# Kernel tuning notes

Measured on AMD Instinct MI355X. Metric: run time of the kernel, lower is better.

The kernel has to match this reference:

```python
import jax, jax.numpy as jnp
import numpy as np

NUM_HEADS = 16
HEAD_SIZE = 64
MAX_POS = 2048  # config.max_position_embeddings


def setup_inputs() -> dict:
    key = jax.random.key(0)
    ks = jax.random.split(key, 8)
    B, Lq, Lk, D = 4, 1024, 2048, 1024
    s = 1.0 / np.sqrt(D)
    return {
        "hidden_states": jax.random.normal(ks[0], (B, Lk, D), jnp.float32),
        "query_hidden_states": jax.random.normal(ks[1], (B, Lq, D), jnp.float32),
        "attention_mask": jnp.zeros((B, 1, 1, Lk), jnp.float32),
        "Wq": jax.random.normal(ks[2], (D, D), jnp.float32) * s,
        "bq": jnp.zeros((D,), jnp.float32),
        "Wk": jax.random.normal(ks[3], (D, D), jnp.float32) * s,
        "bk": jnp.zeros((D,), jnp.float32),
        "Wv": jax.random.normal(ks[4], (D, D), jnp.float32) * s,
        "bv": jnp.zeros((D,), jnp.float32),
        "dist_emb": jax.random.normal(ks[5], (2 * MAX_POS - 1, HEAD_SIZE), jnp.float32) * 0.02,
    }


def _split_heads(x):
    # [B, L, H*Dh] -> [B, H, L, Dh]
    B, L, _ = x.shape
    return x.reshape(B, L, NUM_HEADS, HEAD_SIZE).transpose(0, 2, 1, 3)


def reference(hidden_states, query_hidden_states, attention_mask, Wq, bq, Wk, bk, Wv, bv, dist_emb):
    # Linear projections (torch Linear: x @ W.T + b)
    q = _split_heads(query_hidden_states @ Wq.T + bq)   # [B,H,Lq,Dh]
    k = _split_heads(hidden_states @ Wk.T + bk)          # [B,H,Lk,Dh]
    v = _split_heads(hidden_states @ Wv.T + bv)          # [B,H,Lk,Dh]

    scores = jnp.einsum('bhld,bhrd->bhlr', q, k)         # [B,H,Lq,Lk]

    # relative_key_query positional scores
    Lq, Lk = q.shape[2], k.shape[2]
    distance = jnp.arange(Lq)[:, None] - jnp.arange(Lk)[None, :]
    pe = dist_emb[distance + MAX_POS - 1]                # [Lq,Lk,Dh]
    scores = scores + jnp.einsum('bhld,lrd->bhlr', q, pe) + jnp.einsum('bhrd,lrd->bhlr', k, pe)

    scores = scores / np.sqrt(HEAD_SIZE) + attention_mask
    probs = jax.nn.softmax(scores, axis=-1)              # dropout p=0 (eval)
    ctx = jnp.einsum('bhlr,bhrd->bhld', probs, v)        # [B,H,Lq,Dh]
    B = ctx.shape[0]
    return ctx.transpose(0, 2, 1, 3).reshape(B, Lq, NUM_HEADS * HEAD_SIZE)
```

## Files before the change

### kernel.cpp

```cpp
#include <hip/hip_runtime.h>
#include <hip/hip_bf16.h>

#define B_   4
#define H_   16
#define LQ   1024
#define LK   2048
#define D_   1024
#define DH   64

typedef __attribute__((ext_vector_type(8))) short  short8;
typedef __attribute__((ext_vector_type(4))) float  float4_;
typedef __attribute__((ext_vector_type(4))) unsigned int uint4_;

static __device__ __forceinline__ float bf2f(unsigned short u) {
    unsigned int x = ((unsigned int)u) << 16;
    return __builtin_bit_cast(float, x);
}
static __device__ __forceinline__ unsigned short f2bf(float f) {
    unsigned int x = __builtin_bit_cast(unsigned int, f);
    unsigned int lsb = (x >> 16) & 1u;
    x += 0x7fffu + lsb;
    return (unsigned short)(x >> 16);
}
static __device__ __forceinline__ uint4_ pack8(float4_ a, float4_ b) {
    uint4_ o;
    o[0] = (unsigned int)f2bf(a[0]) | ((unsigned int)f2bf(a[1]) << 16);
    o[1] = (unsigned int)f2bf(a[2]) | ((unsigned int)f2bf(a[3]) << 16);
    o[2] = (unsigned int)f2bf(b[0]) | ((unsigned int)f2bf(b[1]) << 16);
    o[3] = (unsigned int)f2bf(b[2]) | ((unsigned int)f2bf(b[3]) << 16);
    return o;
}

#define MFMA(a, b, c) __builtin_amdgcn_mfma_f32_16x16x32_bf16((a), (b), (c), 0, 0, 0)

__global__ __launch_bounds__(256) void proj_kernel(
    const float* __restrict__ Xq, const float* __restrict__ Xk,
    const float* __restrict__ Wq, const float* __restrict__ bq,
    const float* __restrict__ Wk, const float* __restrict__ bk,
    const float* __restrict__ Wv, const float* __restrict__ bv,
    unsigned short* __restrict__ Qh, unsigned short* __restrict__ Kh,
    unsigned short* __restrict__ VT)
{
    __shared__ short smem[17408];
    short* As = smem;
    short* Bs = smem + 5120;
    short* Cs = smem;

    int bid = blockIdx.x;
    int which, tm, tn;
    const float *X, *W, *bias;
    if (bid < 256)      { which = 0; int t = bid;       tm = t >> 3; tn = t & 7; X = Xq; W = Wq; bias = bq; }
    else if (bid < 768) { which = 1; int t = bid - 256; tm = t >> 3; tn = t & 7; X = Xk; W = Wk; bias = bk; }
    else                { which = 2; int t = bid - 768; tm = t >> 3; tn = t & 7; X = Xk; W = Wv; bias = bv; }

    int tid  = threadIdx.x;
    int wave = tid >> 6, lane = tid & 63;
    int wr = (wave >> 1) * 64, wc = (wave & 1) * 64;
    int m0 = tm * 128, n0 = tn * 128;

    float4_ acc[4][4];
    for (int a = 0; a < 4; ++a) for (int c = 0; c < 4; ++c) acc[a][c] = (float4_)0.0f;

    int srow = tid >> 2, skp = (tid & 3) * 8;
    const float* Ag = X + (size_t)(m0 + srow) * D_ + skp;
    const float* Bg = W + (size_t)(n0 + srow) * D_ + skp;
    int lrow = lane & 15, lk8 = (lane >> 4) * 8;

    for (int kt = 0; kt < 32; ++kt) {
        int k0 = kt * 32;
        for (int i = 0; i < 2; ++i) {
            int row = srow + i * 64;
            const float* pa = Ag + (size_t)i * 64 * D_ + k0;
            const float* pb = Bg + (size_t)i * 64 * D_ + k0;
            float4_ a0 = *(const float4_*)(pa);
            float4_ a1 = *(const float4_*)(pa + 4);
            float4_ b0 = *(const float4_*)(pb);
            float4_ b1 = *(const float4_*)(pb + 4);
            *(uint4_*)(&As[row * 40 + skp]) = pack8(a0, a1);
            *(uint4_*)(&Bs[row * 40 + skp]) = pack8(b0, b1);
        }
        __syncthreads();
        short8 af[4], bfr[4];
        for (int rt = 0; rt < 4; ++rt) af[rt]  = *(const short8*)(&As[(wr + rt * 16 + lrow) * 40 + lk8]);
        for (int ct = 0; ct < 4; ++ct) bfr[ct] = *(const short8*)(&Bs[(wc + ct * 16 + lrow) * 40 + lk8]);
        for (int rt = 0; rt < 4; ++rt)
            for (int ct = 0; ct < 4; ++ct)
                acc[rt][ct] = MFMA(af[rt], bfr[ct], acc[rt][ct]);
        __syncthreads();
    }

    int lrow4 = (lane >> 4) * 4, lcol = lane & 15;
    if (which < 2) {
        int lsh = (which == 0) ? 10 : 11;
        int Lm1 = (1 << lsh) - 1;
        unsigned short* dst = (which == 0) ? Qh : Kh;
        for (int rt = 0; rt < 4; ++rt)
            for (int ct = 0; ct < 4; ++ct)
                for (int i = 0; i < 4; ++i) {
                    int m = m0 + wr + rt * 16 + lrow4 + i;
                    int n = n0 + wc + ct * 16 + lcol;
                    float v = acc[rt][ct][i] + bias[n];
                    int b = m >> lsh, s = m & Lm1;
                    int h = n >> 6, d = n & 63;
                    dst[((size_t)((b * H_ + h) << lsh) + (size_t)s) * DH + d] = f2bf(v);
                }
    } else {
        for (int rt = 0; rt < 4; ++rt)
            for (int ct = 0; ct < 4; ++ct)
                for (int i = 0; i < 4; ++i) {
                    int rl = wr + rt * 16 + lrow4 + i;
                    int cl = wc + ct * 16 + lcol;
                    float v = acc[rt][ct][i] + bias[n0 + cl];
                    Cs[cl * 136 + rl] = (short)f2bf(v);
                }
        __syncthreads();
        int b = m0 >> 11, r0 = m0 & 2047;
        int c = tid >> 1, half = tid & 1;
        int n = n0 + c, h = n >> 6, d = n & 63;
        unsigned short* dstp = VT + ((size_t)(b * H_ + h) * DH + d) * LK + r0 + half * 64;
        for (int j = 0; j < 8; ++j) {
            uint4_ v = *(const uint4_*)(&Cs[c * 136 + half * 64 + j * 8]);
            *(uint4_*)(dstp + j * 8) = v;
        }
    }
}

__global__ __launch_bounds__(256, 2) void attn_kernel(
    const unsigned short* __restrict__ Qh, const unsigned short* __restrict__ Kh,
    const unsigned short* __restrict__ VT, const float* __restrict__ Eg,
    const float* __restrict__ mask, float* __restrict__ out)
{
    __shared__ short smem[32256];
    short* Qs  = smem;
    short* Ks  = smem + 4608;
    short* VTs = smem + 9216;
    short* Es  = smem + 13824;
    short* Ps  = Es;
    short* Gq2 = smem + 23040;
    short* Gk2 = smem + 27648;

    int bid = blockIdx.x;
    int l0 = (bid & 15) * 64;
    int bh = bid >> 4;
    int b  = bh >> 4, h = bh & 15;
    int tid = threadIdx.x, wave = tid >> 6, lane = tid & 63;
    int lrow = lane & 15, lk8 = (lane >> 4) * 8, lrow4 = (lane >> 4) * 4;

    for (int i = 0; i < 2; ++i) {
        int idx = tid + 256 * i, row = idx >> 3, g = (idx & 7) * 8;
        *(uint4_*)(&Qs[row * 72 + g]) =
            *(const uint4_*)(Qh + ((size_t)(bh * LQ + l0 + row)) * DH + g);
    }
    for (int i = tid; i < 2304; i += 256) {
        ((int*)Gq2)[i] = 0;
        ((int*)Gk2)[i] = 0;
    }
    __syncthreads();
    short8 aq0 = *(const short8*)(&Qs[(wave * 16 + lrow) * 72 + lk8]);
    short8 aq1 = *(const short8*)(&Qs[(wave * 16 + lrow) * 72 + 32 + lk8]);

    float m_i[4], l_i[4];
    float4_ Oacc[4];
    for (int i = 0; i < 4; ++i) { m_i[i] = -1e30f; l_i[i] = 0.f; Oacc[i] = (float4_)0.f; }

    for (int it = 0; it < 32; ++it) {
        int r0 = it * 64;
        int jbase = l0 - r0 + 1984;

        for (int i = 0; i < 2; ++i) {
            int idx = tid + 256 * i, row = idx >> 3, g = (idx & 7) * 8;
            *(uint4_*)(&Ks[row * 72 + g]) =
                *(const uint4_*)(Kh + ((size_t)(bh * LK + r0 + row)) * DH + g);
            *(uint4_*)(&VTs[row * 72 + g]) =
                *(const uint4_*)(VT + ((size_t)(bh * DH + row)) * LK + r0 + g);
        }
        for (int i = 0; i < 4; ++i) {
            int idx = tid + 256 * i, row = idx >> 3, g = (idx & 7) * 8;
            const float* pe = Eg + ((size_t)(jbase + row)) * DH + g;
            float4_ e0 = *(const float4_*)(pe);
            float4_ e1 = *(const float4_*)(pe + 4);
            *(uint4_*)(&Es[row * 72 + g]) = pack8(e0, e1);
        }
        __syncthreads();

        float4_ Sacc[4];
        for (int c = 0; c < 4; ++c) {
            short8 b0 = *(const short8*)(&Ks[(c * 16 + lrow) * 72 + lk8]);
            short8 b1 = *(const short8*)(&Ks[(c * 16 + lrow) * 72 + 32 + lk8]);
            float4_ s = (float4_)0.f;
            s = MFMA(aq0, b0, s);
            s = MFMA(aq1, b1, s);
            Sacc[c] = s;
        }

        short8 ak0 = *(const short8*)(&Ks[(wave * 16 + lrow) * 72 + lk8]);
        short8 ak1 = *(const short8*)(&Ks[(wave * 16 + lrow) * 72 + 32 + lk8]);
        float4_ Gq[5], Gk[5];
        for (int tt = 0; tt < 5; ++tt) {
            int tq = wave + tt;
            short8 e0 = *(const short8*)(&Es[(tq * 16 + lrow) * 72 + lk8]);
            short8 e1 = *(const short8*)(&Es[(tq * 16 + lrow) * 72 + 32 + lk8]);
            float4_ g = (float4_)0.f;
            g = MFMA(aq0, e0, g); g = MFMA(aq1, e1, g);
            Gq[tt] = g;
            int tk = (3 - wave) + tt;
            short8 f0 = *(const short8*)(&Es[(tk * 16 + lrow) * 72 + lk8]);
            short8 f1 = *(const short8*)(&Es[(tk * 16 + lrow) * 72 + 32 + lk8]);
            float4_ gg = (float4_)0.f;
            gg = MFMA(ak0, f0, gg); gg = MFMA(ak1, f1, gg);
            Gk[tt] = gg;
        }
        for (int tt = 0; tt < 5; ++tt) {
            int uq = (wave + tt) * 16 + lrow;
            int uk = (3 - wave + tt) * 16 + lrow;
            for (int i = 0; i < 4; ++i) {
                int row = wave * 16 + lrow4 + i;
                int tr = row - uq + 63;
                if (tr >= 0 && tr < 64) Gq2[row * 72 + tr] = (short)f2bf(Gq[tt][i]);
                int tl = uk + row - 63;
                if (tl >= 0 && tl < 64) Gk2[row * 72 + tl] = (short)f2bf(Gk[tt][i]);
            }
        }
        __syncthreads();

        float mk[4];
        for (int c = 0; c < 4; ++c) mk[c] = mask[b * LK + r0 + c * 16 + lrow];
        float p[4][4];
        for (int i = 0; i < 4; ++i) {
            int tl = wave * 16 + lrow4 + i;
            float scv[4], mx = -1e30f;
            for (int c = 0; c < 4; ++c) {
                int tr = c * 16 + lrow;
                float sq = bf2f((unsigned short)Gq2[tl * 72 + tr]);
                float sk = bf2f((unsigned short)Gk2[tr * 72 + tl]);
                float sc = (Sacc[c][i] + sq + sk) * 0.125f + mk[c];
                scv[c] = sc;
                mx = fmaxf(mx, sc);
            }
            for (int off = 1; off < 16; off <<= 1) mx = fmaxf(mx, __shfl_xor(mx, off, 64));
            float mnew = fmaxf(m_i[i], mx);
            float alpha = __expf(m_i[i] - mnew);
            m_i[i] = mnew;
            float rs = 0.f;
            for (int c = 0; c < 4; ++c) {
                float e = __expf(scv[c] - mnew);
                e = bf2f(f2bf(e));
                p[i][c] = e;
                rs += e;
            }
            for (int off = 1; off < 16; off <<= 1) rs += __shfl_xor(rs, off, 64);
            l_i[i] = l_i[i] * alpha + rs;
            for (int nt = 0; nt < 4; ++nt) Oacc[nt][i] *= alpha;
        }
        for (int i = 0; i < 4; ++i) {
            int tl = wave * 16 + lrow4 + i;
            for (int c = 0; c < 4; ++c)
                Ps[tl * 72 + c * 16 + lrow] = (short)f2bf(p[i][c]);
        }
        __asm__ volatile("" ::: "memory");
        short8 ap0 = *(const short8*)(&Ps[(wave * 16 + lrow) * 72 + lk8]);
        short8 ap1 = *(const short8*)(&Ps[(wave * 16 + lrow) * 72 + 32 + lk8]);
        for (int nt = 0; nt < 4; ++nt) {
            short8 v0 = *(const short8*)(&VTs[(nt * 16 + lrow) * 72 + lk8]);
            short8 v1 = *(const short8*)(&VTs[(nt * 16 + lrow) * 72 + 32 + lk8]);
            Oacc[nt] = MFMA(ap0, v0, Oacc[nt]);
            Oacc[nt] = MFMA(ap1, v1, Oacc[nt]);
        }
        __syncthreads();
    }

    for (int nt = 0; nt < 4; ++nt)
        for (int i = 0; i < 4; ++i) {
            int row = l0 + wave * 16 + lrow4 + i;
            int col = h * 64 + nt * 16 + lrow;
            float v = Oacc[nt][i] / l_i[i];
            out[(size_t)(b * LQ + row) * D_ + col] = v;
        }
}

extern "C" void kernel_launch(void* const* d_in, const int* in_sizes, int n_in,
                              void* d_out, int out_size, void* d_ws, size_t ws_size,
                              hipStream_t stream) {
    (void)in_sizes; (void)n_in; (void)out_size; (void)ws_size;
    const float* Xk   = (const float*)d_in[0];
    const float* Xq   = (const float*)d_in[1];
    const float* mask = (const float*)d_in[2];
    const float* Wq   = (const float*)d_in[3];
    const float* bq   = (const float*)d_in[4];
    const float* Wk   = (const float*)d_in[5];
    const float* bk   = (const float*)d_in[6];
    const float* Wv   = (const float*)d_in[7];
    const float* bv   = (const float*)d_in[8];
    const float* Eg   = (const float*)d_in[9];

    unsigned short* Qh = (unsigned short*)d_ws;
    unsigned short* Kh = Qh + (size_t)B_ * H_ * LQ * DH;
    unsigned short* VT = Kh + (size_t)B_ * H_ * LK * DH;
    float* o = (float*)d_out;

    proj_kernel<<<1280, 256, 0, stream>>>(Xq, Xk, Wq, bq, Wk, bk, Wv, bv, Qh, Kh, VT);
    attn_kernel<<<1024, 256, 0, stream>>>(Qh, Kh, VT, Eg, mask, o);
}
```

Baseline: 522.9 us.

## Pre-convert weights and embeddings to bf16, shrink attention LDS for higher occupancy

Adds a conversion kernel that turns Wq/Wk/Wv and the distance embedding into bf16 once per call. The projection and attention kernels then load bf16 directly instead of converting fp32 in their inner loops. The attention kernel cuts its shared memory by aliasing buffers and merging the Gq/Gk tables into one interleaved, XOR-swizzled layout, and raises the launch-bounds occupancy target from 2 to 4. It also drops the per-block zeroing and uses packed bf16 conversion intrinsics, at the cost of an extra kernel launch and extra syncs per iteration.

```diff
diff --git a/kernel.cpp b/kernel.cpp
--- a/kernel.cpp
+++ b/kernel.cpp
@@ -22,22 +22,42 @@
     x += 0x7fffu + lsb;
     return (unsigned short)(x >> 16);
 }
-static __device__ __forceinline__ uint4_ pack8(float4_ a, float4_ b) {
+static __device__ __forceinline__ unsigned int pack2(float a, float b) {
+    __hip_bfloat162 h = __float22bfloat162_rn(make_float2(a, b));
+    unsigned int r;
+    __builtin_memcpy(&r, &h, 4);
+    return r;
+}
+
+#define MFMA(a, b, c) __builtin_amdgcn_mfma_f32_16x16x32_bf16((a), (b), (c), 0, 0, 0)
+
+__global__ __launch_bounds__(256) void conv_kernel(
+    const float* __restrict__ Wq, const float* __restrict__ Wk,
+    const float* __restrict__ Wv, const float* __restrict__ Eg,
+    unsigned short* __restrict__ cWq, unsigned short* __restrict__ cWk,
+    unsigned short* __restrict__ cWv, unsigned short* __restrict__ cEb)
+{
+    int bid = blockIdx.x;
+    const float* src; unsigned short* dst; int nch;
+    if (bid < 512)       { src = Wq; dst = cWq;              nch = 131072; }
+    else if (bid < 1024) { src = Wk; dst = cWk; bid -= 512;  nch = 131072; }
+    else if (bid < 1536) { src = Wv; dst = cWv; bid -= 1024; nch = 131072; }
+    else                 { src = Eg; dst = cEb; bid -= 1536; nch = 32760;  }
+    int ch = bid * 256 + threadIdx.x;
+    if (ch >= nch) return;
+    const float* s = src + (size_t)ch * 8;
+    float4_ v0 = *(const float4_*)s, v1 = *(const float4_*)(s + 4);
     uint4_ o;
-    o[0] = (unsigned int)f2bf(a[0]) | ((unsigned int)f2bf(a[1]) << 16);
-    o[1] = (unsigned int)f2bf(a[2]) | ((unsigned int)f2bf(a[3]) << 16);
-    o[2] = (unsigned int)f2bf(b[0]) | ((unsigned int)f2bf(b[1]) << 16);
-    o[3] = (unsigned int)f2bf(b[2]) | ((unsigned int)f2bf(b[3]) << 16);
-    return o;
-}
-
-#define MFMA(a, b, c) __builtin_amdgcn_mfma_f32_16x16x32_bf16((a), (b), (c), 0, 0, 0)
+    o[0] = pack2(v0[0], v0[1]); o[1] = pack2(v0[2], v0[3]);
+    o[2] = pack2(v1[0], v1[1]); o[3] = pack2(v1[2], v1[3]);
+    *(uint4_*)(dst + (size_t)ch * 8) = o;
+}
 
 __global__ __launch_bounds__(256) void proj_kernel(
     const float* __restrict__ Xq, const float* __restrict__ Xk,
-    const float* __restrict__ Wq, const float* __restrict__ bq,
-    const float* __restrict__ Wk, const float* __restrict__ bk,
-    const float* __restrict__ Wv, const float* __restrict__ bv,
+    const unsigned short* __restrict__ Wq, const float* __restrict__ bq,
+    const unsigned short* __restrict__ Wk, const float* __restrict__ bk,
+    const unsigned short* __restrict__ Wv, const float* __restrict__ bv,
     unsigned short* __restrict__ Qh, unsigned short* __restrict__ Kh,
     unsigned short* __restrict__ VT)
 {
@@ -48,7 +68,7 @@
 
     int bid = blockIdx.x;
     int which, tm, tn;
-    const float *X, *W, *bias;
+    const float *X, *bias; const unsigned short* W;
     if (bid < 256)      { which = 0; int t = bid;       tm = t >> 3; tn = t & 7; X = Xq; W = Wq; bias = bq; }
     else if (bid < 768) { which = 1; int t = bid - 256; tm = t >> 3; tn = t & 7; X = Xk; W = Wk; bias = bk; }
     else                { which = 2; int t = bid - 768; tm = t >> 3; tn = t & 7; X = Xk; W = Wv; bias = bv; }
@@ -62,8 +82,8 @@
     for (int a = 0; a < 4; ++a) for (int c = 0; c < 4; ++c) acc[a][c] = (float4_)0.0f;
 
     int srow = tid >> 2, skp = (tid & 3) * 8;
-    const float* Ag = X + (size_t)(m0 + srow) * D_ + skp;
-    const float* Bg = W + (size_t)(n0 + srow) * D_ + skp;
+    const float*          Ag = X + (size_t)(m0 + srow) * D_ + skp;
+    const unsigned short* Bg = W + (size_t)(n0 + srow) * D_ + skp;
     int lrow = lane & 15, lk8 = (lane >> 4) * 8;
 
     for (int kt = 0; kt < 32; ++kt) {
@@ -71,13 +91,14 @@
         for (int i = 0; i < 2; ++i) {
             int row = srow + i * 64;
             const float* pa = Ag + (size_t)i * 64 * D_ + k0;
-            const float* pb = Bg + (size_t)i * 64 * D_ + k0;
             float4_ a0 = *(const float4_*)(pa);
             float4_ a1 = *(const float4_*)(pa + 4);
-            float4_ b0 = *(const float4_*)(pb);
-            float4_ b1 = *(const float4_*)(pb + 4);
-            *(uint4_*)(&As[row * 40 + skp]) = pack8(a0, a1);
-            *(uint4_*)(&Bs[row * 40 + skp]) = pack8(b0, b1);
+            uint4_ va;
+            va[0] = pack2(a0[0], a0[1]); va[1] = pack2(a0[2], a0[3]);
+            va[2] = pack2(a1[0], a1[1]); va[3] = pack2(a1[2], a1[3]);
+            uint4_ vb = *(const uint4_*)(Bg + (size_t)i * 64 * D_ + k0);
+            *(uint4_*)(&As[row * 40 + skp]) = va;
+            *(uint4_*)(&Bs[row * 40 + skp]) = vb;
         }
         __syncthreads();
         short8 af[4], bfr[4];
@@ -125,114 +146,116 @@
     }
 }
 
-__global__ __launch_bounds__(256, 2) void attn_kernel(
+__global__ __launch_bounds__(256, 4) void attn_kernel(
     const unsigned short* __restrict__ Qh, const unsigned short* __restrict__ Kh,
-    const unsigned short* __restrict__ VT, const float* __restrict__ Eg,
+    const unsigned short* __restrict__ VT, const unsigned short* __restrict__ Eb,
     const float* __restrict__ mask, float* __restrict__ out)
 {
-    __shared__ short smem[32256];
+    __shared__ short smem[18432];
     short* Qs  = smem;
-    short* Ks  = smem + 4608;
-    short* VTs = smem + 9216;
-    short* Es  = smem + 13824;
-    short* Ps  = Es;
-    short* Gq2 = smem + 23040;
-    short* Gk2 = smem + 27648;
+    short* Ks  = smem;
+    short* VTs = smem + 4608;
+    short* Es  = smem + 9216;
+    short* G2  = smem + 9216;
 
     int bid = blockIdx.x;
     int l0 = (bid & 15) * 64;
     int bh = bid >> 4;
     int b  = bh >> 4, h = bh & 15;
     int tid = threadIdx.x, wave = tid >> 6, lane = tid & 63;
-    int lrow = lane & 15, lk8 = (lane >> 4) * 8, lrow4 = (lane >> 4) * 4;
+    int lr = lane & 15, lk8 = (lane >> 4) * 8, lr4 = (lane >> 4) * 4;
 
     for (int i = 0; i < 2; ++i) {
         int idx = tid + 256 * i, row = idx >> 3, g = (idx & 7) * 8;
         *(uint4_*)(&Qs[row * 72 + g]) =
             *(const uint4_*)(Qh + ((size_t)(bh * LQ + l0 + row)) * DH + g);
     }
-    for (int i = tid; i < 2304; i += 256) {
-        ((int*)Gq2)[i] = 0;
-        ((int*)Gk2)[i] = 0;
-    }
     __syncthreads();
-    short8 aq0 = *(const short8*)(&Qs[(wave * 16 + lrow) * 72 + lk8]);
-    short8 aq1 = *(const short8*)(&Qs[(wave * 16 + lrow) * 72 + 32 + lk8]);
+    short8 aq0 = *(const short8*)(&Qs[(wave * 16 + lr) * 72 + lk8]);
+    short8 aq1 = *(const short8*)(&Qs[(wave * 16 + lr) * 72 + 32 + lk8]);
 
     float m_i[4], l_i[4];
     float4_ Oacc[4];
     for (int i = 0; i < 4; ++i) { m_i[i] = -1e30f; l_i[i] = 0.f; Oacc[i] = (float4_)0.f; }
 
+    const unsigned short* Kbase = Kh + (size_t)bh * LK * DH;
+    const unsigned short* Vbase = VT + (size_t)bh * DH * LK;
+
     for (int it = 0; it < 32; ++it) {
         int r0 = it * 64;
         int jbase = l0 - r0 + 1984;
 
+        __syncthreads();
         for (int i = 0; i < 2; ++i) {
             int idx = tid + 256 * i, row = idx >> 3, g = (idx & 7) * 8;
             *(uint4_*)(&Ks[row * 72 + g]) =
-                *(const uint4_*)(Kh + ((size_t)(bh * LK + r0 + row)) * DH + g);
+                *(const uint4_*)(Kbase + (size_t)(r0 + row) * DH + g);
             *(uint4_*)(&VTs[row * 72 + g]) =
-                *(const uint4_*)(VT + ((size_t)(bh * DH + row)) * LK + r0 + g);
+                *(const uint4_*)(Vbase + (size_t)row * LK + r0 + g);
         }
         for (int i = 0; i < 4; ++i) {
             int idx = tid + 256 * i, row = idx >> 3, g = (idx & 7) * 8;
-            const float* pe = Eg + ((size_t)(jbase + row)) * DH + g;
-            float4_ e0 = *(const float4_*)(pe);
-            float4_ e1 = *(const float4_*)(pe + 4);
-            *(uint4_*)(&Es[row * 72 + g]) = pack8(e0, e1);
+            *(uint4_*)(&Es[row * 72 + g]) =
+                *(const uint4_*)(Eb + (size_t)(jbase + row) * DH + g);
         }
         __syncthreads();
 
         float4_ Sacc[4];
         for (int c = 0; c < 4; ++c) {
-            short8 b0 = *(const short8*)(&Ks[(c * 16 + lrow) * 72 + lk8]);
-            short8 b1 = *(const short8*)(&Ks[(c * 16 + lrow) * 72 + 32 + lk8]);
+            short8 b0 = *(const short8*)(&Ks[(c * 16 + lr) * 72 + lk8]);
+            short8 b1 = *(const short8*)(&Ks[(c * 16 + lr) * 72 + 32 + lk8]);
             float4_ s = (float4_)0.f;
             s = MFMA(aq0, b0, s);
             s = MFMA(aq1, b1, s);
             Sacc[c] = s;
         }
 
-        short8 ak0 = *(const short8*)(&Ks[(wave * 16 + lrow) * 72 + lk8]);
-        short8 ak1 = *(const short8*)(&Ks[(wave * 16 + lrow) * 72 + 32 + lk8]);
-        float4_ Gq[5], Gk[5];
+        short8 ak0 = *(const short8*)(&Ks[(wave * 16 + lr) * 72 + lk8]);
+        short8 ak1 = *(const short8*)(&Ks[(wave * 16 + lr) * 72 + 32 + lk8]);
+        unsigned int gqp[5][2], gkp[5][2];
         for (int tt = 0; tt < 5; ++tt) {
             int tq = wave + tt;
-            short8 e0 = *(const short8*)(&Es[(tq * 16 + lrow) * 72 + lk8]);
-            short8 e1 = *(const short8*)(&Es[(tq * 16 + lrow) * 72 + 32 + lk8]);
+            short8 e0 = *(const short8*)(&Es[(tq * 16 + lr) * 72 + lk8]);
+            short8 e1 = *(const short8*)(&Es[(tq * 16 + lr) * 72 + 32 + lk8]);
             float4_ g = (float4_)0.f;
             g = MFMA(aq0, e0, g); g = MFMA(aq1, e1, g);
-            Gq[tt] = g;
+            gqp[tt][0] = pack2(g[0], g[1]); gqp[tt][1] = pack2(g[2], g[3]);
             int tk = (3 - wave) + tt;
-            short8 f0 = *(const short8*)(&Es[(tk * 16 + lrow) * 72 + lk8]);
-            short8 f1 = *(const short8*)(&Es[(tk * 16 + lrow) * 72 + 32 + lk8]);
+            short8 f0 = *(const short8*)(&Es[(tk * 16 + lr) * 72 + lk8]);
+            short8 f1 = *(const short8*)(&Es[(tk * 16 + lr) * 72 + 32 + lk8]);
             float4_ gg = (float4_)0.f;
             gg = MFMA(ak0, f0, gg); gg = MFMA(ak1, f1, gg);
-            Gk[tt] = gg;
-        }
+            gkp[tt][0] = pack2(gg[0], gg[1]); gkp[tt][1] = pack2(gg[2], gg[3]);
+        }
+        __syncthreads();
+
         for (int tt = 0; tt < 5; ++tt) {
-            int uq = (wave + tt) * 16 + lrow;
-            int uk = (3 - wave + tt) * 16 + lrow;
+            int uq = (wave + tt) * 16 + lr;
+            int uk = (3 - wave + tt) * 16 + lr;
             for (int i = 0; i < 4; ++i) {
-                int row = wave * 16 + lrow4 + i;
+                int row = wave * 16 + lr4 + i;
+                unsigned int wq32 = gqp[tt][i >> 1], wk32 = gkp[tt][i >> 1];
+                unsigned short vq = (unsigned short)((i & 1) ? (wq32 >> 16) : (wq32 & 0xffff));
+                unsigned short vk = (unsigned short)((i & 1) ? (wk32 >> 16) : (wk32 & 0xffff));
                 int tr = row - uq + 63;
-                if (tr >= 0 && tr < 64) Gq2[row * 72 + tr] = (short)f2bf(Gq[tt][i]);
+                if ((unsigned)tr < 64u)
+                    G2[row * 144 + (((tr & 15) ^ (row & 7)) << 3) + ((tr >> 4) << 1)] = (short)vq;
                 int tl = uk + row - 63;
-                if (tl >= 0 && tl < 64) Gk2[row * 72 + tl] = (short)f2bf(Gk[tt][i]);
+                if ((unsigned)tl < 64u)
+                    G2[tl * 144 + (((row & 15) ^ (tl & 7)) << 3) + ((row >> 4) << 1) + 1] = (short)vk;
             }
         }
         __syncthreads();
 
         float mk[4];
-        for (int c = 0; c < 4; ++c) mk[c] = mask[b * LK + r0 + c * 16 + lrow];
-        float p[4][4];
+        for (int c = 0; c < 4; ++c) mk[c] = mask[b * LK + r0 + c * 16 + lr];
         for (int i = 0; i < 4; ++i) {
-            int tl = wave * 16 + lrow4 + i;
+            int tl = wave * 16 + lr4 + i;
+            short8 gv = *(const short8*)(&G2[tl * 144 + ((lr ^ (tl & 7)) << 3)]);
             float scv[4], mx = -1e30f;
             for (int c = 0; c < 4; ++c) {
-                int tr = c * 16 + lrow;
-                float sq = bf2f((unsigned short)Gq2[tl * 72 + tr]);
-                float sk = bf2f((unsigned short)Gk2[tr * 72 + tl]);
+                float sq = bf2f((unsigned short)gv[2 * c]);
+                float sk = bf2f((unsigned short)gv[2 * c + 1]);
                 float sc = (Sacc[c][i] + sq + sk) * 0.125f + mk[c];
                 scv[c] = sc;
                 mx = fmaxf(mx, sc);
@@ -241,40 +264,34 @@
             float mnew = fmaxf(m_i[i], mx);
             float alpha = __expf(m_i[i] - mnew);
             m_i[i] = mnew;
-            float rs = 0.f;
-            for (int c = 0; c < 4; ++c) {
-                float e = __expf(scv[c] - mnew);
-                e = bf2f(f2bf(e));
-                p[i][c] = e;
-                rs += e;
-            }
+            float e0 = __expf(scv[0] - mnew), e1 = __expf(scv[1] - mnew);
+            float e2 = __expf(scv[2] - mnew), e3 = __expf(scv[3] - mnew);
+            unsigned int p01 = pack2(e0, e1), p23 = pack2(e2, e3);
+            float rs = bf2f((unsigned short)(p01 & 0xffff)) + bf2f((unsigned short)(p01 >> 16))
+                     + bf2f((unsigned short)(p23 & 0xffff)) + bf2f((unsigned short)(p23 >> 16));
             for (int off = 1; off < 16; off <<= 1) rs += __shfl_xor(rs, off, 64);
             l_i[i] = l_i[i] * alpha + rs;
             for (int nt = 0; nt < 4; ++nt) Oacc[nt][i] *= alpha;
-        }
-        for (int i = 0; i < 4; ++i) {
-            int tl = wave * 16 + lrow4 + i;
-            for (int c = 0; c < 4; ++c)
-                Ps[tl * 72 + c * 16 + lrow] = (short)f2bf(p[i][c]);
-        }
-        __asm__ volatile("" ::: "memory");
-        short8 ap0 = *(const short8*)(&Ps[(wave * 16 + lrow) * 72 + lk8]);
-        short8 ap1 = *(const short8*)(&Ps[(wave * 16 + lrow) * 72 + 32 + lk8]);
+            G2[tl * 144 +  0 + lr] = (short)(unsigned short)(p01 & 0xffff);
+            G2[tl * 144 + 16 + lr] = (short)(unsigned short)(p01 >> 16);
+            G2[tl * 144 + 32 + lr] = (short)(unsigned short)(p23 & 0xffff);
+            G2[tl * 144 + 48 + lr] = (short)(unsigned short)(p23 >> 16);
+        }
+        short8 ap0 = *(const short8*)(&G2[(wave * 16 + lr) * 144 + lk8]);
+        short8 ap1 = *(const short8*)(&G2[(wave * 16 + lr) * 144 + 32 + lk8]);
         for (int nt = 0; nt < 4; ++nt) {
-            short8 v0 = *(const short8*)(&VTs[(nt * 16 + lrow) * 72 + lk8]);
-            short8 v1 = *(const short8*)(&VTs[(nt * 16 + lrow) * 72 + 32 + lk8]);
+            short8 v0 = *(const short8*)(&VTs[(nt * 16 + lr) * 72 + lk8]);
+            short8 v1 = *(const short8*)(&VTs[(nt * 16 + lr) * 72 + 32 + lk8]);
             Oacc[nt] = MFMA(ap0, v0, Oacc[nt]);
             Oacc[nt] = MFMA(ap1, v1, Oacc[nt]);
         }
-        __syncthreads();
     }
 
     for (int nt = 0; nt < 4; ++nt)
         for (int i = 0; i < 4; ++i) {
-            int row = l0 + wave * 16 + lrow4 + i;
-            int col = h * 64 + nt * 16 + lrow;
-            float v = Oacc[nt][i] / l_i[i];
-            out[(size_t)(b * LQ + row) * D_ + col] = v;
+            int row = l0 + wave * 16 + lr4 + i;
+            int col = h * 64 + nt * 16 + lr;
+            out[(size_t)(b * LQ + row) * D_ + col] = Oacc[nt][i] / l_i[i];
         }
 }
 
@@ -293,11 +310,16 @@
     const float* bv   = (const float*)d_in[8];
     const float* Eg   = (const float*)d_in[9];
 
-    unsigned short* Qh = (unsigned short*)d_ws;
-    unsigned short* Kh = Qh + (size_t)B_ * H_ * LQ * DH;
-    unsigned short* VT = Kh + (size_t)B_ * H_ * LK * DH;
+    unsigned short* Qh  = (unsigned short*)d_ws;
+    unsigned short* Kh  = Qh  + (size_t)4194304;
+    unsigned short* VT  = Kh  + (size_t)8388608;
+    unsigned short* cWq = VT  + (size_t)8388608;
+    unsigned short* cWk = cWq + (size_t)1048576;
+    unsigned short* cWv = cWk + (size_t)1048576;
+    unsigned short* cEb = cWv + (size_t)1048576;
     float* o = (float*)d_out;
 
-    proj_kernel<<<1280, 256, 0, stream>>>(Xq, Xk, Wq, bq, Wk, bk, Wv, bv, Qh, Kh, VT);
-    attn_kernel<<<1024, 256, 0, stream>>>(Qh, Kh, VT, Eg, mask, o);
-}
+    conv_kernel<<<1664, 256, 0, stream>>>(Wq, Wk, Wv, Eg, cWq, cWk, cWv, cEb);
+    proj_kernel<<<1280, 256, 0, stream>>>(Xq, Xk, cWq, bq, cWk, bk, cWv, bv, Qh, Kh, VT);
+    attn_kernel<<<1024, 256, 0, stream>>>(Qh, Kh, VT, cEb, mask, o);
+}
```

Result: slower. 944.3 us (+80.6%).
